# Performance work log

Measured on AMD Instinct MI355X. Metric: run time of the kernel, lower is better.

## Reference

```python
import jax, jax.numpy as jnp
import numpy as np
from jax import lax

B, D, C, K = 8192, 512, 1000, 8
EPS = 1e-8
TEMP = 0.2
NEG = -10000.0


def setup_inputs() -> dict:
    key = jax.random.key(0)
    ks = jax.random.split(key, 6)
    z = jax.random.normal(ks[0], (B, D), dtype=jnp.float32)
    n_exp = jax.random.randint(ks[1], (B,), 0, K, dtype=jnp.int32)
    s1 = 1.0 / np.sqrt(D)
    W1 = jax.random.normal(ks[2], (K, D, D), dtype=jnp.float32) * s1
    b1 = jax.random.normal(ks[3], (K, D), dtype=jnp.float32) * 0.01
    W2 = jax.random.normal(ks[4], (K, D, C), dtype=jnp.float32) * s1
    b2 = jax.random.normal(ks[5], (K, C), dtype=jnp.float32) * 0.01
    return {"z": z, "n_exp": n_exp, "W1": W1, "b1": b1, "W2": W2, "b2": b2}


def _gates_one(p, c, n):
    # p: [K,C] softmax probs for one sample; c: [K] confidences; n: scalar int
    pn = p / (jnp.linalg.norm(p, axis=-1, keepdims=True) + EPS)
    S = pn @ pn.T  # [K,K] pairwise cosine similarity
    sel0 = jnp.zeros((K,), dtype=bool).at[jnp.argmax(c)].set(True)

    def body(t, sel):
        # max cosine sim of each candidate to already-selected set
        max_sim = jnp.max(jnp.where(sel[None, :], S, -jnp.inf), axis=1)
        dist = jnp.where(sel, -jnp.inf, 1.0 - max_sim)
        new = sel.at[jnp.argmax(dist)].set(True)
        return jnp.where(t < n, new, sel)

    sel = lax.fori_loop(1, K, body, sel0)
    gate_logits = jnp.where(sel, c, NEG) / TEMP
    return jax.nn.softmax(gate_logits)


def reference(z, n_exp, W1, b1, W2, b2):
    # K expert MLPs, batched: [B,d] -> [B,K,C]
    h = jax.nn.relu(jnp.einsum('bd,kde->bke', z, W1) + b1[None])
    logits_all = jnp.einsum('bke,kec->bkc', h, W2) + b2[None]
    probs = jax.nn.softmax(logits_all, axis=-1)
    conf = jnp.max(probs, axis=-1)  # [B,K]
    gates = jax.vmap(_gates_one)(probs, conf, n_exp)  # [B,K]
    logits = jnp.einsum('bkc,bk->bc', logits_all, gates)
    return logits, gates
```

## Files before the change

kernel.cpp:

```cpp
#include <hip/hip_runtime.h>
#include <math.h>

#define B_SZ 8192
#define D_DIM 512
#define C_DIM 1000
#define C_PAD 1024
#define K_EXP 8
#define TEMP_INV 5.0f
#define EPS_N 1e-8f

typedef __attribute__((ext_vector_type(8))) short frag_ab;
typedef __attribute__((ext_vector_type(4))) float frag_cd;

__device__ __forceinline__ short f2bf(float f) {
    unsigned u = __builtin_bit_cast(unsigned, f);
    unsigned r = (u + 0x7fffu + ((u >> 16) & 1u)) >> 16;
    return (short)r;
}
__device__ __forceinline__ float bf2f(short s) {
    unsigned u = ((unsigned)(unsigned short)s) << 16;
    return __builtin_bit_cast(float, u);
}
__device__ __forceinline__ void split2(float v, short& s0, short& s1) {
    s0 = f2bf(v);
    s1 = f2bf(v - bf2f(s0));
}

__device__ __forceinline__ void gl_lds16(const short* g, short* l) {
    __builtin_amdgcn_global_load_lds(
        (const __attribute__((address_space(1))) unsigned int*)(const void*)g,
        (__attribute__((address_space(3))) unsigned int*)(void*)l,
        16, 0, 0);
}

__global__ __launch_bounds__(256) void prep_z(const float* __restrict__ z,
                                              short* __restrict__ p0, short* __restrict__ p1) {
    int idx = blockIdx.x * 256 + threadIdx.x;
    float v = z[idx];
    short a, b; split2(v, a, b);
    p0[idx] = a; p1[idx] = b;
}

__global__ __launch_bounds__(256) void prep_w1t(const float* __restrict__ W1,
                                                short* __restrict__ p0, short* __restrict__ p1) {
    __shared__ float t[32][33];
    const int k = blockIdx.z;
    const int d0 = blockIdx.x * 32;
    const int e0 = blockIdx.y * 32;
    const int tx = threadIdx.x & 31, ty = threadIdx.x >> 5;
    const float* src = W1 + ((size_t)k << 18);
#pragma unroll
    for (int r = 0; r < 4; r++) {
        int d = d0 + ty + 8 * r;
        t[ty + 8 * r][tx] = src[(size_t)d * 512 + e0 + tx];
    }
    __syncthreads();
#pragma unroll
    for (int r = 0; r < 4; r++) {
        int e = e0 + ty + 8 * r;
        int d = d0 + tx;
        float v = t[tx][ty + 8 * r];
        short a, b; split2(v, a, b);
        size_t o = ((size_t)k << 18) + (size_t)e * 512 + d;
        p0[o] = a; p1[o] = b;
    }
}

__global__ __launch_bounds__(256) void prep_w2t(const float* __restrict__ W2,
                                                short* __restrict__ p0, short* __restrict__ p1) {
    __shared__ float t[32][33];
    const int k = blockIdx.z;
    const int e0 = blockIdx.x * 32;
    const int c0 = blockIdx.y * 32;
    const int tx = threadIdx.x & 31, ty = threadIdx.x >> 5;
    const float* src = W2 + (size_t)k * (D_DIM * C_DIM);
#pragma unroll
    for (int r = 0; r < 4; r++) {
        int e = e0 + ty + 8 * r;
        int c = c0 + tx;
        t[ty + 8 * r][tx] = (c < C_DIM) ? src[(size_t)e * C_DIM + c] : 0.f;
    }
    __syncthreads();
#pragma unroll
    for (int r = 0; r < 4; r++) {
        int c = c0 + ty + 8 * r;
        int e = e0 + tx;
        float v = t[tx][ty + 8 * r];
        short a, b; split2(v, a, b);
        size_t o = (size_t)k * (C_PAD * D_DIM) + (size_t)c * 512 + e;
        p0[o] = a; p1[o] = b;
    }
}

__global__ __launch_bounds__(512, 2) void gemm_split(
    const short* __restrict__ A0, const short* __restrict__ A1, long long aBatch,
    const short* __restrict__ B0, const short* __restrict__ B1, long long bBatch,
    const float* __restrict__ bias, int biasBatch,
    float* __restrict__ Cf, long long cBatch, int ldc, int Nout,
    short* __restrict__ H0, short* __restrict__ H1, long long hBatch,
    int mt, int nt, int mode)
{
    const int lin = blockIdx.x;
    const int k = lin & 7;
    const int rem = lin >> 3;
    const int gm = (mt >= 2) ? 2 : 1;
    const int win = rem / (gm * nt);
    const int local = rem % (gm * nt);
    const int m0 = (win * gm + local / nt) * 256;
    const int n0 = (local % nt) * 256;

    const int tid = threadIdx.x;
    const int lane = tid & 63;
    const int wv = tid >> 6;
    const int wm = (wv & 1) * 128;
    const int wn = (wv >> 1) * 64;

    __shared__ short lds[65536];
    short* ldsA = lds;
    short* ldsB = lds + 32768;

    const short* aP0 = A0 + (size_t)k * aBatch + (size_t)m0 * 512;
    const short* aP1 = A1 + (size_t)k * aBatch + (size_t)m0 * 512;
    const short* bP0 = B0 + (size_t)k * bBatch + (size_t)n0 * 512;
    const short* bP1 = B1 + (size_t)k * bBatch + (size_t)n0 * 512;

    frag_cd acc[8][4];
#pragma unroll
    for (int i = 0; i < 8; i++)
#pragma unroll
        for (int j = 0; j < 4; j++)
            acc[i][j] = (frag_cd){0.f, 0.f, 0.f, 0.f};

    const int srow = tid >> 2;
    const int sc   = tid & 3;
    const int q    = lane >> 4;
    const int rb   = lane & 15;

#define SROW_STAGE(gsrc, ldst, KK0) do {                                        \
    _Pragma("unroll")                                                           \
    for (int hh = 0; hh < 2; hh++) {                                            \
        int row = hh * 128 + srow;                                              \
        int gq = sc ^ ((row >> 1) & 3);                                         \
        gl_lds16((gsrc) + (size_t)row * 512 + (KK0) + gq * 8,                   \
                 (ldst) + row * 32 + sc * 8);                                   \
    }                                                                           \
} while (0)

#define READ_B(BUFC) do {                                                       \
    _Pragma("unroll")                                                           \
    for (int j = 0; j < 4; j++) {                                               \
        int R = wn + j * 16 + rb;                                               \
        int slot = q ^ ((R >> 1) & 3);                                          \
        bfr0[j] = *(const frag_ab*)(ldsB + (BUFC) + R * 32 + slot * 8);         \
        bfr1[j] = *(const frag_ab*)(ldsB + (BUFC) + 8192 + R * 32 + slot * 8);  \
    }                                                                           \
} while (0)

#define READ_A(DST, P, BUFC) do {                                               \
    _Pragma("unroll")                                                           \
    for (int ii = 0; ii < 2; ii++) {                                            \
        int R = wm + ((P) * 2 + ii) * 16 + rb;                                  \
        int slot = q ^ ((R >> 1) & 3);                                          \
        DST[ii][0] = *(const frag_ab*)(ldsA + (BUFC) + R * 32 + slot * 8);      \
        DST[ii][1] = *(const frag_ab*)(ldsA + (BUFC) + 8192 + R * 32 + slot * 8);\
    }                                                                           \
} while (0)

#define MFMA_Q(P, AR) do {                                                      \
    __builtin_amdgcn_s_setprio(1);                                              \
    _Pragma("unroll")                                                           \
    for (int ii = 0; ii < 2; ii++)                                              \
        _Pragma("unroll")                                                       \
        for (int j = 0; j < 4; j++) {                                           \
            frag_cd c = acc[(P) * 2 + ii][j];                                   \
            c = __builtin_amdgcn_mfma_f32_16x16x32_bf16(AR[ii][0], bfr0[j], c, 0, 0, 0); \
            c = __builtin_amdgcn_mfma_f32_16x16x32_bf16(AR[ii][0], bfr1[j], c, 0, 0, 0); \
            c = __builtin_amdgcn_mfma_f32_16x16x32_bf16(AR[ii][1], bfr0[j], c, 0, 0, 0); \
            acc[(P) * 2 + ii][j] = c;                                           \
        }                                                                       \
    __builtin_amdgcn_s_setprio(0);                                              \
} while (0)

#define PH_BAR() do {                                                           \
    __builtin_amdgcn_sched_barrier(0);                                          \
    __builtin_amdgcn_s_barrier();                                               \
    __builtin_amdgcn_sched_barrier(0);                                          \
} while (0)

    SROW_STAGE(bP0, ldsB + 0,            0);
    SROW_STAGE(bP1, ldsB + 8192,         0);
    SROW_STAGE(aP0, ldsA + 0,            0);
    SROW_STAGE(aP1, ldsA + 8192,         0);
    SROW_STAGE(bP0, ldsB + 16384,        32);
    SROW_STAGE(bP1, ldsB + 16384 + 8192, 32);
    asm volatile("s_waitcnt vmcnt(4)" ::: "memory");
    PH_BAR();

    auto kstep = [&](int T, bool s01, bool s23, int vmn) __attribute__((always_inline)) {
        const int bufc = (T & 1) * 16384;
        const int nb1  = ((T + 1) & 1) * 16384;
        const int kk1  = (T + 1) * 32;
        const int kk2  = (T + 2) * 32;
        frag_ab bfr0[4], bfr1[4];
        frag_ab aC[2][2], aN[2][2];

        READ_B(bufc);
        READ_A(aC, 0, bufc);
        READ_A(aN, 1, bufc);
        if (s01) SROW_STAGE(aP0, ldsA + nb1, kk1);
        MFMA_Q(0, aC);
        PH_BAR();

        READ_A(aC, 2, bufc);
        if (s01) SROW_STAGE(aP1, ldsA + nb1 + 8192, kk1);
        MFMA_Q(1, aN);
        PH_BAR();

        READ_A(aN, 3, bufc);
        if (s23) SROW_STAGE(bP0, ldsB + bufc, kk2);
        MFMA_Q(2, aC);
        PH_BAR();

        if (s23) SROW_STAGE(bP1, ldsB + bufc + 8192, kk2);
        MFMA_Q(3, aN);
        if (vmn == 4)      asm volatile("s_waitcnt vmcnt(4)" ::: "memory");
        else if (vmn == 0) asm volatile("s_waitcnt vmcnt(0)" ::: "memory");
        PH_BAR();
    };

    for (int t = 0; t < 14; ++t) kstep(t, true, true, 4);
    kstep(14, true, false, 0);
    kstep(15, false, false, -1);

#undef SROW_STAGE
#undef READ_B
#undef READ_A
#undef MFMA_Q
#undef PH_BAR

    const int r0 = (lane >> 4) * 4;
    const int cc = lane & 15;
    if (mode == 0) {
        float* C = Cf + (size_t)k * cBatch;
        const float* bb = bias + (size_t)k * biasBatch;
#pragma unroll
        for (int i = 0; i < 8; i++) {
            int rowb = m0 + wm + i * 16 + r0;
#pragma unroll
            for (int j = 0; j < 4; j++) {
                int col = n0 + wn + j * 16 + cc;
                if (col < Nout) {
                    float b = bb[col];
#pragma unroll
                    for (int r = 0; r < 4; r++)
                        C[(size_t)(rowb + r) * ldc + col] = acc[i][j][r] + b;
                }
            }
        }
    } else {
        short* h0 = H0 + (size_t)k * hBatch;
        short* h1 = H1 + (size_t)k * hBatch;
        const float* bb = bias + (size_t)k * biasBatch;
#pragma unroll
        for (int i = 0; i < 8; i++) {
            int rowb = m0 + wm + i * 16 + r0;
#pragma unroll
            for (int j = 0; j < 4; j++) {
                int col = n0 + wn + j * 16 + cc;
                float b = bb[col];
#pragma unroll
                for (int r = 0; r < 4; r++) {
                    float v = fmaxf(acc[i][j][r] + b, 0.f);
                    short s0, s1; split2(v, s0, s1);
                    size_t o = (size_t)(rowb + r) * 512 + col;
                    h0[o] = s0; h1[o] = s1;
                }
            }
        }
    }
}

__global__ __launch_bounds__(256) void gate_combine(
    const float* __restrict__ L,
    const int* __restrict__ n_exp,
    float* __restrict__ out_logits,
    float* __restrict__ out_gates,
    int Bc)
{
    const int wv = threadIdx.x >> 6;
    const int lane = threadIdx.x & 63;
    const int b = blockIdx.x * 4 + wv;
    const size_t kcs = (size_t)Bc * C_DIM;
    const float* Lb = L + (size_t)b * C_DIM;

    __shared__ float Sm[4][64];
    __shared__ float Zm[4][8];

    float mx[K_EXP], Zs[K_EXP], dd[36];
#pragma unroll
    for (int k = 0; k < K_EXP; k++) { mx[k] = -INFINITY; Zs[k] = 0.f; }
#pragma unroll
    for (int p = 0; p < 36; p++) dd[p] = 0.f;

    for (int c = lane; c < C_DIM; c += 64) {
        float e[K_EXP];
#pragma unroll
        for (int k = 0; k < K_EXP; k++) {
            float l = Lb[(size_t)k * kcs + c];
            mx[k] = fmaxf(mx[k], l);
            e[k] = __expf(l);
            Zs[k] += e[k];
        }
        int idx = 0;
#pragma unroll
        for (int i = 0; i < K_EXP; i++)
#pragma unroll
            for (int j = i; j < K_EXP; j++) {
                dd[idx] = fmaf(e[i], e[j], dd[idx]);
                idx++;
            }
    }

#pragma unroll
    for (int off = 32; off > 0; off >>= 1) {
#pragma unroll
        for (int k = 0; k < K_EXP; k++) {
            mx[k] = fmaxf(mx[k], __shfl_xor(mx[k], off, 64));
            Zs[k] += __shfl_xor(Zs[k], off, 64);
        }
#pragma unroll
        for (int p = 0; p < 36; p++)
            dd[p] += __shfl_xor(dd[p], off, 64);
    }

    if (lane == 0) {
        int idx = 0;
#pragma unroll
        for (int i = 0; i < K_EXP; i++)
#pragma unroll
            for (int j = i; j < K_EXP; j++) {
                Sm[wv][i * 8 + j] = dd[idx];
                Sm[wv][j * 8 + i] = dd[idx];
                idx++;
            }
#pragma unroll
        for (int k = 0; k < K_EXP; k++) Zm[wv][k] = Zs[k];
    }

    const int ti = lane >> 3, tj = lane & 7;
    const float Zi = Zm[wv][ti], Zj = Zm[wv][tj];
    const float dij = Sm[wv][ti * 8 + tj];
    const float dii = Sm[wv][ti * 8 + ti];
    const float djj = Sm[wv][tj * 8 + tj];
    const float ni = sqrtf(dii) / Zi + EPS_N;
    const float nj = sqrtf(djj) / Zj + EPS_N;
    const float cosij = (dij / (Zi * Zj)) / (ni * nj);

    float conf[K_EXP];
#pragma unroll
    for (int k = 0; k < K_EXP; k++) conf[k] = __expf(mx[k]) / Zs[k];

    int i0 = 0; float bcf = conf[0];
#pragma unroll
    for (int k = 1; k < K_EXP; k++)
        if (conf[k] > bcf) { bcf = conf[k]; i0 = k; }
    unsigned sel = 1u << i0;
    const int n = n_exp[b];

    for (int t = 1; t < K_EXP; t++) {
        float v = ((sel >> tj) & 1u) ? cosij : -INFINITY;
        v = fmaxf(v, __shfl_xor(v, 1, 64));
        v = fmaxf(v, __shfl_xor(v, 2, 64));
        v = fmaxf(v, __shfl_xor(v, 4, 64));
        float dist = ((sel >> ti) & 1u) ? -INFINITY : 1.0f - v;
        float bv = dist; int bi = ti;
#pragma unroll
        for (int off = 8; off < 64; off <<= 1) {
            float ov = __shfl_xor(bv, off, 64);
            int oi = __shfl_xor(bi, off, 64);
            if (ov > bv || (ov == bv && oi < bi)) { bv = ov; bi = oi; }
        }
        if (t < n) sel |= 1u << bi;
    }

    float cmax = -INFINITY;
#pragma unroll
    for (int k = 0; k < K_EXP; k++)
        if ((sel >> k) & 1u) cmax = fmaxf(cmax, conf[k]);
    float g[K_EXP], gsum = 0.f;
#pragma unroll
    for (int k = 0; k < K_EXP; k++) {
        g[k] = ((sel >> k) & 1u) ? __expf((conf[k] - cmax) * TEMP_INV) : 0.f;
        gsum += g[k];
    }
    const float ginv = 1.0f / gsum;
#pragma unroll
    for (int k = 0; k < K_EXP; k++) g[k] *= ginv;

    if (lane == 0) {
        float4* og = (float4*)(out_gates + (size_t)b * K_EXP);
        og[0] = make_float4(g[0], g[1], g[2], g[3]);
        og[1] = make_float4(g[4], g[5], g[6], g[7]);
    }

    for (int c = lane; c < C_DIM; c += 64) {
        float o = 0.f;
#pragma unroll
        for (int k = 0; k < K_EXP; k++)
            o = fmaf(g[k], Lb[(size_t)k * kcs + c], o);
        out_logits[(size_t)b * C_DIM + c] = o;
    }
}

extern "C" void kernel_launch(void* const* d_in, const int* in_sizes, int n_in,
                              void* d_out, int out_size, void* d_ws, size_t ws_size,
                              hipStream_t stream) {
    const float* z     = (const float*)d_in[0];
    const int*   n_exp = (const int*)d_in[1];
    const float* W1    = (const float*)d_in[2];
    const float* b1    = (const float*)d_in[3];
    const float* W2    = (const float*)d_in[4];
    const float* b2    = (const float*)d_in[5];
    float* out_logits = (float*)d_out;
    float* out_gates  = (float*)d_out + (size_t)B_SZ * C_DIM;

    const size_t zP   = (size_t)B_SZ * D_DIM * 2;
    const size_t w1P  = (size_t)K_EXP * D_DIM * D_DIM * 2;
    const size_t w2P  = (size_t)K_EXP * C_PAD * D_DIM * 2;
    const size_t fixedBytes = 2 * (zP + w1P + w2P);

    int nch = 1;
    while (nch < 32 && fixedBytes + (size_t)(B_SZ / nch) * 48384 > ws_size) nch *= 2;
    const int Bc = B_SZ / nch;

    char* w = (char*)d_ws;
    short* zp[2];  zp[0]  = (short*)w; zp[1]  = (short*)(w + zP);  w += 2 * zP;
    short* w1t[2]; w1t[0] = (short*)w; w1t[1] = (short*)(w + w1P); w += 2 * w1P;
    short* w2t[2]; w2t[0] = (short*)w; w2t[1] = (short*)(w + w2P); w += 2 * w2P;
    const size_t hP = (size_t)K_EXP * Bc * D_DIM * 2;
    short* hp[2];  hp[0]  = (short*)w; hp[1]  = (short*)(w + hP);  w += 2 * hP;
    float* Lb = (float*)w;

    prep_z <<<dim3((B_SZ * D_DIM) / 256), 256, 0, stream>>>(z, zp[0], zp[1]);
    prep_w1t<<<dim3(16, 16, K_EXP), 256, 0, stream>>>(W1, w1t[0], w1t[1]);
    prep_w2t<<<dim3(16, 32, K_EXP), 256, 0, stream>>>(W2, w2t[0], w2t[1]);

    const int mt = Bc / 256;

    for (int ch = 0; ch < nch; ch++) {
        const int off = ch * Bc;
        const long long zoff = (long long)off * D_DIM;

        gemm_split<<<dim3(8 * mt * 2), 512, 0, stream>>>(
            zp[0] + zoff, zp[1] + zoff, 0LL,
            w1t[0], w1t[1], (long long)D_DIM * D_DIM,
            b1, D_DIM,
            nullptr, 0LL, 0, D_DIM,
            hp[0], hp[1], (long long)Bc * D_DIM,
            mt, 2, 1);

        gemm_split<<<dim3(8 * mt * 4), 512, 0, stream>>>(
            hp[0], hp[1], (long long)Bc * D_DIM,
            w2t[0], w2t[1], (long long)C_PAD * D_DIM,
            b2, C_DIM,
            Lb, (long long)Bc * C_DIM, C_DIM, C_DIM,
            nullptr, nullptr, 0LL,
            mt, 4, 0);

        gate_combine<<<dim3(Bc / 4), 256, 0, stream>>>(
            Lb, n_exp + off,
            out_logits + (size_t)off * C_DIM,
            out_gates + (size_t)off * K_EXP,
            Bc);
    }
}
```

Before: 485.6 us.

## Store logits sample-major and give each sample a block with register-held float4 loads

The second GEMM now writes its logits as [B][K][C] instead of [K][B][C], so each sample's 8x1000 values sit in one contiguous block. gate_combine launches one 256-thread block per sample. 250 threads each load float4 slices for all experts once, keep them in registers, and reduce across waves through shared memory. The combine step reuses those registers instead of reading the logits from global memory a second time. The cost is a block-wide sync, a serial gating section on one wave, and four times as many blocks.

After: 550.8 us. 13.4% more time.

```diff
diff --git a/kernel.cpp b/kernel.cpp
--- a/kernel.cpp
+++ b/kernel.cpp
@@ -287,36 +287,41 @@
     float* __restrict__ out_gates,
     int Bc)
 {
-    const int wv = threadIdx.x >> 6;
-    const int lane = threadIdx.x & 63;
-    const int b = blockIdx.x * 4 + wv;
-    const size_t kcs = (size_t)Bc * C_DIM;
-    const float* Lb = L + (size_t)b * C_DIM;
-
-    __shared__ float Sm[4][64];
-    __shared__ float Zm[4][8];
-
+    const int b = blockIdx.x;
+    const int tid = threadIdx.x;
+    const int wv = tid >> 6;
+    const int lane = tid & 63;
+    const bool act = tid < (C_DIM / 4);
+    const float* Lb = L + (size_t)b * (K_EXP * C_DIM);
+
+    __shared__ float partial[4][52];
+    __shared__ float gsh[K_EXP];
+
+    float4 lv[K_EXP];
     float mx[K_EXP], Zs[K_EXP], dd[36];
 #pragma unroll
     for (int k = 0; k < K_EXP; k++) { mx[k] = -INFINITY; Zs[k] = 0.f; }
 #pragma unroll
     for (int p = 0; p < 36; p++) dd[p] = 0.f;
 
-    for (int c = lane; c < C_DIM; c += 64) {
-        float e[K_EXP];
+    if (act) {
+        float e[K_EXP][4];
 #pragma unroll
         for (int k = 0; k < K_EXP; k++) {
-            float l = Lb[(size_t)k * kcs + c];
-            mx[k] = fmaxf(mx[k], l);
-            e[k] = __expf(l);
-            Zs[k] += e[k];
+            lv[k] = *(const float4*)(Lb + k * C_DIM + tid * 4);
+            mx[k] = fmaxf(fmaxf(lv[k].x, lv[k].y), fmaxf(lv[k].z, lv[k].w));
+            e[k][0] = __expf(lv[k].x); e[k][1] = __expf(lv[k].y);
+            e[k][2] = __expf(lv[k].z); e[k][3] = __expf(lv[k].w);
+            Zs[k] = (e[k][0] + e[k][1]) + (e[k][2] + e[k][3]);
         }
         int idx = 0;
 #pragma unroll
         for (int i = 0; i < K_EXP; i++)
 #pragma unroll
             for (int j = i; j < K_EXP; j++) {
-                dd[idx] = fmaf(e[i], e[j], dd[idx]);
+                dd[idx] = fmaf(e[i][0], e[j][0],
+                          fmaf(e[i][1], e[j][1],
+                          fmaf(e[i][2], e[j][2], e[i][3] * e[j][3])));
                 idx++;
             }
     }
@@ -332,83 +337,111 @@
         for (int p = 0; p < 36; p++)
             dd[p] += __shfl_xor(dd[p], off, 64);
     }
-
     if (lane == 0) {
-        int idx = 0;
-#pragma unroll
-        for (int i = 0; i < K_EXP; i++)
-#pragma unroll
-            for (int j = i; j < K_EXP; j++) {
-                Sm[wv][i * 8 + j] = dd[idx];
-                Sm[wv][j * 8 + i] = dd[idx];
-                idx++;
+#pragma unroll
+        for (int k = 0; k < K_EXP; k++) { partial[wv][k] = mx[k]; partial[wv][8 + k] = Zs[k]; }
+#pragma unroll
+        for (int p = 0; p < 36; p++) partial[wv][16 + p] = dd[p];
+    }
+    __syncthreads();
+
+    if (wv == 0) {
+#pragma unroll
+        for (int k = 0; k < K_EXP; k++) {
+            mx[k] = fmaxf(fmaxf(partial[0][k], partial[1][k]),
+                          fmaxf(partial[2][k], partial[3][k]));
+            Zs[k] = (partial[0][8 + k] + partial[1][8 + k]) +
+                    (partial[2][8 + k] + partial[3][8 + k]);
+        }
+#pragma unroll
+        for (int p = 0; p < 36; p++)
+            dd[p] = (partial[0][16 + p] + partial[1][16 + p]) +
+                    (partial[2][16 + p] + partial[3][16 + p]);
+
+        const int ti = lane >> 3, tj = lane & 7;
+        float S[K_EXP][K_EXP];
+        {
+            int idx = 0;
+#pragma unroll
+            for (int i = 0; i < K_EXP; i++)
+#pragma unroll
+                for (int j = i; j < K_EXP; j++) {
+                    S[i][j] = dd[idx]; S[j][i] = dd[idx];
+                    idx++;
+                }
+        }
+        const float Zi = Zs[ti], Zj = Zs[tj];
+        const float dij = S[ti][tj];
+        const float dii = S[ti][ti];
+        const float djj = S[tj][tj];
+        const float ni = sqrtf(dii) / Zi + EPS_N;
+        const float nj = sqrtf(djj) / Zj + EPS_N;
+        const float cosij = (dij / (Zi * Zj)) / (ni * nj);
+
+        float conf[K_EXP];
+#pragma unroll
+        for (int k = 0; k < K_EXP; k++) conf[k] = __expf(mx[k]) / Zs[k];
+
+        int i0 = 0; float bcf = conf[0];
+#pragma unroll
+        for (int k = 1; k < K_EXP; k++)
+            if (conf[k] > bcf) { bcf = conf[k]; i0 = k; }
+        unsigned sel = 1u << i0;
+        const int n = n_exp[b];
+
+        for (int t = 1; t < K_EXP; t++) {
+            float v = ((sel >> tj) & 1u) ? cosij : -INFINITY;
+            v = fmaxf(v, __shfl_xor(v, 1, 64));
+            v = fmaxf(v, __shfl_xor(v, 2, 64));
+            v = fmaxf(v, __shfl_xor(v, 4, 64));
+            float dist = ((sel >> ti) & 1u) ? -INFINITY : 1.0f - v;
+            float bv = dist; int bi = ti;
+#pragma unroll
+            for (int off = 8; off < 64; off <<= 1) {
+                float ov = __shfl_xor(bv, off, 64);
+                int oi = __shfl_xor(bi, off, 64);
+                if (ov > bv || (ov == bv && oi < bi)) { bv = ov; bi = oi; }
             }
-#pragma unroll
-        for (int k = 0; k < K_EXP; k++) Zm[wv][k] = Zs[k];
-    }
-
-    const int ti = lane >> 3, tj = lane & 7;
-    const float Zi = Zm[wv][ti], Zj = Zm[wv][tj];
-    const float dij = Sm[wv][ti * 8 + tj];
-    const float dii = Sm[wv][ti * 8 + ti];
-    const float djj = Sm[wv][tj * 8 + tj];
-    const float ni = sqrtf(dii) / Zi + EPS_N;
-    const float nj = sqrtf(djj) / Zj + EPS_N;
-    const float cosij = (dij / (Zi * Zj)) / (ni * nj);
-
-    float conf[K_EXP];
-#pragma unroll
-    for (int k = 0; k < K_EXP; k++) conf[k] = __expf(mx[k]) / Zs[k];
-
-    int i0 = 0; float bcf = conf[0];
-#pragma unroll
-    for (int k = 1; k < K_EXP; k++)
-        if (conf[k] > bcf) { bcf = conf[k]; i0 = k; }
-    unsigned sel = 1u << i0;
-    const int n = n_exp[b];
-
-    for (int t = 1; t < K_EXP; t++) {
-        float v = ((sel >> tj) & 1u) ? cosij : -INFINITY;
-        v = fmaxf(v, __shfl_xor(v, 1, 64));
-        v = fmaxf(v, __shfl_xor(v, 2, 64));
-        v = fmaxf(v, __shfl_xor(v, 4, 64));
-        float dist = ((sel >> ti) & 1u) ? -INFINITY : 1.0f - v;
-        float bv = dist; int bi = ti;
-#pragma unroll
-        for (int off = 8; off < 64; off <<= 1) {
-            float ov = __shfl_xor(bv, off, 64);
-            int oi = __shfl_xor(bi, off, 64);
-            if (ov > bv || (ov == bv && oi < bi)) { bv = ov; bi = oi; }
-        }
-        if (t < n) sel |= 1u << bi;
-    }
-
-    float cmax = -INFINITY;
-#pragma unroll
-    for (int k = 0; k < K_EXP; k++)
-        if ((sel >> k) & 1u) cmax = fmaxf(cmax, conf[k]);
-    float g[K_EXP], gsum = 0.f;
-#pragma unroll
-    for (int k = 0; k < K_EXP; k++) {
-        g[k] = ((sel >> k) & 1u) ? __expf((conf[k] - cmax) * TEMP_INV) : 0.f;
-        gsum += g[k];
-    }
-    const float ginv = 1.0f / gsum;
-#pragma unroll
-    for (int k = 0; k < K_EXP; k++) g[k] *= ginv;
-
-    if (lane == 0) {
-        float4* og = (float4*)(out_gates + (size_t)b * K_EXP);
-        og[0] = make_float4(g[0], g[1], g[2], g[3]);
-        og[1] = make_float4(g[4], g[5], g[6], g[7]);
-    }
-
-    for (int c = lane; c < C_DIM; c += 64) {
-        float o = 0.f;
+            if (t < n) sel |= 1u << bi;
+        }
+
+        float cmax = -INFINITY;
 #pragma unroll
         for (int k = 0; k < K_EXP; k++)
-            o = fmaf(g[k], Lb[(size_t)k * kcs + c], o);
-        out_logits[(size_t)b * C_DIM + c] = o;
+            if ((sel >> k) & 1u) cmax = fmaxf(cmax, conf[k]);
+        float g[K_EXP], gsum = 0.f;
+#pragma unroll
+        for (int k = 0; k < K_EXP; k++) {
+            g[k] = ((sel >> k) & 1u) ? __expf((conf[k] - cmax) * TEMP_INV) : 0.f;
+            gsum += g[k];
+        }
+        const float ginv = 1.0f / gsum;
+#pragma unroll
+        for (int k = 0; k < K_EXP; k++) g[k] *= ginv;
+
+        if (lane == 0) {
+#pragma unroll
+            for (int k = 0; k < K_EXP; k++) gsh[k] = g[k];
+            float4* og = (float4*)(out_gates + (size_t)b * K_EXP);
+            og[0] = make_float4(g[0], g[1], g[2], g[3]);
+            og[1] = make_float4(g[4], g[5], g[6], g[7]);
+        }
+    }
+    __syncthreads();
+
+    if (act) {
+        float g[K_EXP];
+#pragma unroll
+        for (int k = 0; k < K_EXP; k++) g[k] = gsh[k];
+        float4 o = make_float4(0.f, 0.f, 0.f, 0.f);
+#pragma unroll
+        for (int k = 0; k < K_EXP; k++) {
+            o.x = fmaf(g[k], lv[k].x, o.x);
+            o.y = fmaf(g[k], lv[k].y, o.y);
+            o.z = fmaf(g[k], lv[k].z, o.z);
+            o.w = fmaf(g[k], lv[k].w, o.w);
+        }
+        *(float4*)(out_logits + (size_t)b * C_DIM + tid * 4) = o;
     }
 }
 
@@ -463,11 +496,11 @@
             hp[0], hp[1], (long long)Bc * D_DIM,
             w2t[0], w2t[1], (long long)C_PAD * D_DIM,
             b2, C_DIM,
-            Lb, (long long)Bc * C_DIM, C_DIM, C_DIM,
+            Lb, (long long)C_DIM, K_EXP * C_DIM, C_DIM,
             nullptr, nullptr, 0LL,
             mt, 4, 0);
 
-        gate_combine<<<dim3(Bc / 4), 256, 0, stream>>>(
+        gate_combine<<<dim3(Bc), 256, 0, stream>>>(
             Lb, n_exp + off,
             out_logits + (size_t)off * C_DIM,
             out_gates + (size_t)off * K_EXP,
```
